# Optimization experiments

Measured on AMD Instinct MI355X. Metric: run time of the kernel, lower is better.

## Reference

```python
import jax, jax.numpy as jnp
import numpy as np
import math

B, S, D, H = 4, 2048, 512, 8
DK = D // H
EPS = 1e-6

def _xavier(key, shape):
    fan_in, fan_out = shape[1], shape[0]
    a = math.sqrt(6.0 / (fan_in + fan_out))
    return jax.random.uniform(key, shape, jnp.float32, -a, a)

def setup_inputs() -> dict:
    key = jax.random.key(0)
    ks = jax.random.split(key, 8)
    return {
        "x_q": jax.random.normal(ks[0], (B, S, D), jnp.float32),
        "x_k": jax.random.normal(ks[1], (B, S, D), jnp.float32),
        "Wq": _xavier(ks[2], (D, D)),
        "Wk": _xavier(ks[3], (D, D)),
        "Wv": _xavier(ks[4], (D, D)),
        "Wg": jnp.zeros((D, D), jnp.float32),      # gating weight init to 0
        "bg": jnp.ones((D,), jnp.float32),          # gating bias init to 1
        "Wo": _xavier(ks[5], (D, D)),
        "bo": jnp.zeros((D,), jnp.float32),
        "gamma": jnp.ones((D,), jnp.float32),
        "beta": jnp.zeros((D,), jnp.float32),
    }

def _ln(x, gamma, beta):
    mu = jnp.mean(x, axis=-1, keepdims=True)
    var = jnp.var(x, axis=-1, keepdims=True)
    return (x - mu) * jax.lax.rsqrt(var + EPS) * gamma + beta

def reference(x_q, x_k, Wq, Wk, Wv, Wg, bg, Wo, bo, gamma, beta):
    xq = _ln(x_q, gamma, beta)          # [B,S,D]
    xk = _ln(x_k, gamma, beta)
    q = xq @ Wq.T                        # nn.Linear: x @ W^T (no bias)
    k = xk @ Wk.T
    v = xk @ Wv.T
    q = q.reshape(B, S, H, DK)
    k = k.reshape(B, S, H, DK)
    v = v.reshape(B, S, H, DK)
    attn = jnp.einsum('bshd,bthd->bhst', q, k) / math.sqrt(DK)  # [B,H,S,S]
    attn = jax.nn.softmax(attn, axis=-1) * jax.nn.softmax(attn, axis=-2)
    out = jnp.einsum('bhst,bthd->bshd', attn, v).reshape(B, S, D)
    gate = jax.nn.sigmoid(xq @ Wg.T + bg)
    return (out * gate) @ Wo.T + bo
```

## Files before the change

kernel.cpp:

```cpp
#include <hip/hip_runtime.h>

#define BB 4
#define SS 2048
#define DD 512
#define HH 8
#define RR (BB * SS)
#define BH (BB * HH)

typedef unsigned short u16;
typedef unsigned int   u32;
typedef __attribute__((ext_vector_type(4))) float f32x4;
typedef __attribute__((ext_vector_type(8))) short bf16x8;

__device__ __forceinline__ float bf2f(u16 u) { return __uint_as_float(((u32)u) << 16); }
__device__ __forceinline__ u16 f2bf(float f) {
    u32 x = __float_as_uint(f);
    return (u16)((x + 0x7fffu + ((x >> 16) & 1u)) >> 16);
}
__device__ __forceinline__ bool is_bf16(const void* gamma) {
    return *(const u32*)gamma == 0x3F803F80u;
}
__device__ __forceinline__ float ldin(const void* p, size_t i, bool b16) {
    return b16 ? bf2f(((const u16*)p)[i]) : ((const float*)p)[i];
}
__device__ __forceinline__ float expc(float x) { return __expf(fminf(x, 60.f)); }

__global__ __launch_bounds__(256) void k_ln(
    const void* xq, const void* xk, const void* gamma, const void* beta,
    u16* __restrict__ lnq, u16* __restrict__ lnk, float* l_col)
{
    bool b16 = is_bf16(gamma);
    int row = blockIdx.x, tid = threadIdx.x;
    const void* x = blockIdx.y ? xk : xq;
    u16* o = blockIdx.y ? lnk : lnq;
    size_t base = (size_t)row * DD;

    if (blockIdx.y == 0 && row < 256) l_col[row * 256 + tid] = 0.f;

    float x0 = ldin(x, base + tid * 2, b16);
    float x1 = ldin(x, base + tid * 2 + 1, b16);
    float s = x0 + x1, ss = x0 * x0 + x1 * x1;
    for (int m = 1; m < 64; m <<= 1) { s += __shfl_xor(s, m); ss += __shfl_xor(ss, m); }
    __shared__ float ws4[4], wss4[4], mu_s, rs_s;
    int wv = tid >> 6;
    if ((tid & 63) == 0) { ws4[wv] = s; wss4[wv] = ss; }
    __syncthreads();
    if (tid == 0) {
        float S1 = ws4[0] + ws4[1] + ws4[2] + ws4[3];
        float S2 = wss4[0] + wss4[1] + wss4[2] + wss4[3];
        float mu = S1 / (float)DD;
        float var = S2 / (float)DD - mu * mu;
        mu_s = mu; rs_s = rsqrtf(fmaxf(var, 0.f) + 1e-6f);
    }
    __syncthreads();
    float mu = mu_s, rstd = rs_s;
    float g0 = ldin(gamma, tid * 2, b16), g1 = ldin(gamma, tid * 2 + 1, b16);
    float b0 = ldin(beta, tid * 2, b16),  b1 = ldin(beta, tid * 2 + 1, b16);
    o[base + tid * 2]     = f2bf((x0 - mu) * rstd * g0 + b0);
    o[base + tid * 2 + 1] = f2bf((x1 - mu) * rstd * g1 + b1);
}

__global__ __launch_bounds__(256) void k_proj4(
    const u16* __restrict__ lnq, const u16* __restrict__ lnk,
    const void* Wq, const void* Wk, const void* Wv, const void* Wg,
    const void* bg, const void* gamma,
    u16* __restrict__ qb, u16* __restrict__ kb,
    u16* __restrict__ vT, u16* __restrict__ gb)
{
    __shared__ __align__(16) u16 As[128][64];
    __shared__ __align__(16) u16 Bs[128][64];
    bool b16 = is_bf16(gamma);
    int which = blockIdx.z;
    const u16* A = (which <= 1) ? lnq : lnk;
    const void* W = (which == 0) ? Wq : (which == 1) ? Wg : (which == 2) ? Wk : Wv;
    u16* C = (which == 0) ? qb : (which == 1) ? gb : (which == 2) ? kb : vT;

    int tid = threadIdx.x;
    int lane = tid & 63, wave = tid >> 6;
    int r = lane & 15, q4 = lane >> 4;
    int m0 = blockIdx.y * 128, n0 = blockIdx.x * 128;
    int moff = (wave >> 1) * 64, noff = (wave & 1) * 64;
    const int K = DD, N = DD;

    f32x4 acc[4][4];
    for (int i = 0; i < 4; ++i)
        for (int j = 0; j < 4; ++j) acc[i][j] = (f32x4){0.f, 0.f, 0.f, 0.f};

    for (int k0 = 0; k0 < K; k0 += 64) {
        #pragma unroll
        for (int t = 0; t < 4; ++t) {
            int e = t * 2048 + tid * 8;
            int row = e >> 6, kk = e & 63;
            int ksw = kk ^ ((row & 7) * 8);
            *(uint4*)&As[row][ksw] = *(const uint4*)&A[(size_t)(m0 + row) * K + k0 + kk];
            if (b16) {
                *(uint4*)&Bs[row][ksw] =
                    *(const uint4*)&((const u16*)W)[(size_t)(n0 + row) * K + k0 + kk];
            } else {
                const float* wp = (const float*)W + (size_t)(n0 + row) * K + k0 + kk;
                float4 w0 = *(const float4*)wp;
                float4 w1 = *(const float4*)(wp + 4);
                ushort4 lo, hi;
                lo.x = f2bf(w0.x); lo.y = f2bf(w0.y); lo.z = f2bf(w0.z); lo.w = f2bf(w0.w);
                hi.x = f2bf(w1.x); hi.y = f2bf(w1.y); hi.z = f2bf(w1.z); hi.w = f2bf(w1.w);
                *(ushort4*)&Bs[row][ksw] = lo;
                *(ushort4*)&Bs[row][ksw + 4] = hi;
            }
        }
        __syncthreads();
        #pragma unroll
        for (int ksp = 0; ksp < 2; ++ksp) {
            int kb2 = ksp * 32 + q4 * 8;
            bf16x8 af[4], bfr[4];
            #pragma unroll
            for (int i = 0; i < 4; ++i) {
                int rowm = moff + i * 16 + r;
                af[i] = *(const bf16x8*)&As[rowm][kb2 ^ ((rowm & 7) * 8)];
                int rown = noff + i * 16 + r;
                bfr[i] = *(const bf16x8*)&Bs[rown][kb2 ^ ((rown & 7) * 8)];
            }
            #pragma unroll
            for (int i = 0; i < 4; ++i)
                #pragma unroll
                for (int j = 0; j < 4; ++j)
                    acc[i][j] = __builtin_amdgcn_mfma_f32_16x16x32_bf16(af[i], bfr[j], acc[i][j], 0, 0, 0);
        }
        __syncthreads();
    }

    if (which == 3) {
        int b = m0 >> 11;
        int sb = (m0 & 2047) + moff + q4 * 4;
        #pragma unroll
        for (int j = 0; j < 4; ++j) {
            int n = n0 + noff + j * 16 + r;
            int h = n >> 6, dkl = n & 63;
            size_t vbase = (((size_t)b * 8 + h) * 64 + dkl) * SS;
            #pragma unroll
            for (int i = 0; i < 4; ++i) {
                ushort4 wv;
                wv.x = f2bf(acc[i][j][0]); wv.y = f2bf(acc[i][j][1]);
                wv.z = f2bf(acc[i][j][2]); wv.w = f2bf(acc[i][j][3]);
                *(ushort4*)&C[vbase + sb + i * 16] = wv;
            }
        }
    } else {
        #pragma unroll
        for (int j = 0; j < 4; ++j) {
            int col = n0 + noff + j * 16 + r;
            float bj = (which == 1) ? ldin(bg, col, b16) : 0.f;
            #pragma unroll
            for (int i = 0; i < 4; ++i) {
                int rowb = m0 + moff + i * 16 + q4 * 4;
                #pragma unroll
                for (int g = 0; g < 4; ++g) {
                    float v = acc[i][j][g];
                    if (which == 1) v = 1.f / (1.f + expc(-(v + bj)));
                    C[(size_t)(rowb + g) * N + col] = f2bf(v);
                }
            }
        }
    }
}

__global__ __launch_bounds__(256) void k_sum(
    const u16* __restrict__ qm, const u16* __restrict__ km,
    float* __restrict__ l_row, float* __restrict__ l_col)
{
    __shared__ __align__(16) u16 Qs[64][64];
    __shared__ __align__(16) u16 Ks[128][64];
    __shared__ float colS[128];
    int tid = threadIdx.x, lane = tid & 63, wave = tid >> 6;
    int r = lane & 15, q4 = lane >> 4;
    int s0 = blockIdx.x * 64;
    int bh = blockIdx.y, b = bh >> 3, h = bh & 7;
    size_t hb = (size_t)b * SS * DD + (size_t)h * 64;

    #pragma unroll
    for (int t = 0; t < 2; ++t) {
        int e = t * 2048 + tid * 8;
        int row = e >> 6, kk = e & 63;
        *(uint4*)&Qs[row][kk ^ ((row & 7) * 8)] = *(const uint4*)&qm[hb + (size_t)(s0 + row) * DD + kk];
    }
    if (tid < 128) colS[tid] = 0.f;
    __syncthreads();

    int moff = wave * 16;
    bf16x8 aq[2];
    #pragma unroll
    for (int ksp = 0; ksp < 2; ++ksp) {
        int rowm = moff + r;
        aq[ksp] = *(const bf16x8*)&Qs[rowm][(ksp * 32 + q4 * 8) ^ ((rowm & 7) * 8)];
    }

    float rs[4] = {};
    for (int t0 = 0; t0 < SS; t0 += 128) {
        #pragma unroll
        for (int t = 0; t < 4; ++t) {
            int e = t * 2048 + tid * 8;
            int row = e >> 6, kk = e & 63;
            *(uint4*)&Ks[row][kk ^ ((row & 7) * 8)] = *(const uint4*)&km[hb + (size_t)(t0 + row) * DD + kk];
        }
        __syncthreads();

        f32x4 acc[8];
        for (int j = 0; j < 8; ++j) acc[j] = (f32x4){0.f, 0.f, 0.f, 0.f};
        #pragma unroll
        for (int ksp = 0; ksp < 2; ++ksp) {
            int kb2 = ksp * 32 + q4 * 8;
            bf16x8 bk[8];
            #pragma unroll
            for (int j = 0; j < 8; ++j) {
                int n = j * 16 + r;
                bk[j] = *(const bf16x8*)&Ks[n][kb2 ^ ((n & 7) * 8)];
            }
            #pragma unroll
            for (int j = 0; j < 8; ++j)
                acc[j] = __builtin_amdgcn_mfma_f32_16x16x32_bf16(aq[ksp], bk[j], acc[j], 0, 0, 0);
        }

        float cv[8];
        #pragma unroll
        for (int j = 0; j < 8; ++j) {
            cv[j] = 0.f;
            #pragma unroll
            for (int g = 0; g < 4; ++g) {
                float ev = expc(acc[j][g] * 0.125f);
                rs[g] += ev;
                cv[j] += ev;
            }
        }
        #pragma unroll
        for (int j = 0; j < 8; ++j) {
            float v = cv[j];
            v += __shfl_xor(v, 16); v += __shfl_xor(v, 32);
            if (q4 == 0) atomicAdd(&colS[j * 16 + r], v);
        }
        __syncthreads();
        if (tid < 128) {
            atomicAdd(&l_col[(size_t)bh * SS + t0 + tid], colS[tid]);
            colS[tid] = 0.f;
        }
        __syncthreads();
    }
    #pragma unroll
    for (int g = 0; g < 4; ++g) {
        float v = rs[g];
        v += __shfl_xor(v, 1); v += __shfl_xor(v, 2);
        v += __shfl_xor(v, 4); v += __shfl_xor(v, 8);
        if (r == 0) l_row[(size_t)bh * SS + s0 + moff + q4 * 4 + g] = v;
    }
}

__global__ void k_rcp(const float* __restrict__ l_row, const float* __restrict__ l_col,
                      float* __restrict__ inv_r, float* __restrict__ inv_c, int n)
{
    int i = blockIdx.x * blockDim.x + threadIdx.x;
    if (i < n) {
        inv_r[i] = 1.f / fmaxf(l_row[i], 1e-30f);
        inv_c[i] = 1.f / fmaxf(l_col[i], 1e-30f);
    }
}

__global__ __launch_bounds__(256) void k_pv(
    const u16* __restrict__ qm, const u16* __restrict__ km, const u16* __restrict__ vT,
    const float* __restrict__ inv_r, const float* __restrict__ inv_c,
    const u16* __restrict__ gate, u16* __restrict__ og)
{
    __shared__ __align__(16) u16 Ep[64][128];
    __shared__ __align__(16) u16 KV[8192];
    int tid = threadIdx.x, lane = tid & 63, wave = tid >> 6;
    int r = lane & 15, q4 = lane >> 4;
    int s0 = blockIdx.x * 64;
    int bh = blockIdx.y, b = bh >> 3, h = bh & 7;
    size_t hb = (size_t)b * SS * DD + (size_t)h * 64;
    int moff = wave * 16;

    #pragma unroll
    for (int t = 0; t < 2; ++t) {
        int e = t * 2048 + tid * 8;
        int row = e >> 6, kk = e & 63;
        *(uint4*)&Ep[row][kk ^ ((row & 7) * 8)] = *(const uint4*)&qm[hb + (size_t)(s0 + row) * DD + kk];
    }
    __syncthreads();
    bf16x8 aq[2];
    #pragma unroll
    for (int ksp = 0; ksp < 2; ++ksp) {
        int rowm = moff + r;
        aq[ksp] = *(const bf16x8*)&Ep[rowm][(ksp * 32 + q4 * 8) ^ ((rowm & 7) * 8)];
    }
    __syncthreads();

    f32x4 acco[4];
    for (int j = 0; j < 4; ++j) acco[j] = (f32x4){0.f, 0.f, 0.f, 0.f};

    for (int t0 = 0; t0 < SS; t0 += 128) {
        #pragma unroll
        for (int t = 0; t < 4; ++t) {
            int e = t * 2048 + tid * 8;
            int row = e >> 6, kk = e & 63;
            *(uint4*)&KV[row * 64 + (kk ^ ((row & 7) * 8))] =
                *(const uint4*)&km[hb + (size_t)(t0 + row) * DD + kk];
        }
        __syncthreads();

        f32x4 accs[8];
        for (int j = 0; j < 8; ++j) accs[j] = (f32x4){0.f, 0.f, 0.f, 0.f};
        #pragma unroll
        for (int ksp = 0; ksp < 2; ++ksp) {
            int kb2 = ksp * 32 + q4 * 8;
            bf16x8 bk[8];
            #pragma unroll
            for (int j = 0; j < 8; ++j) {
                int n = j * 16 + r;
                bk[j] = *(const bf16x8*)&KV[n * 64 + (kb2 ^ ((n & 7) * 8))];
            }
            #pragma unroll
            for (int j = 0; j < 8; ++j)
                accs[j] = __builtin_amdgcn_mfma_f32_16x16x32_bf16(aq[ksp], bk[j], accs[j], 0, 0, 0);
        }
        __syncthreads();

        #pragma unroll
        for (int c = 0; c < 4; ++c) {
            int e = c * 256 + tid;
            int row = e >> 4, tc = (e & 15) * 8;
            *(uint4*)&KV[row * 128 + (tc ^ ((row & 7) * 8))] =
                *(const uint4*)&vT[((size_t)bh * 64 + row) * SS + t0 + tc];
        }
        #pragma unroll
        for (int j = 0; j < 8; ++j) {
            float icj = inv_c[(size_t)bh * SS + t0 + j * 16 + r];
            int srow = moff + q4 * 4;
            #pragma unroll
            for (int g = 0; g < 4; ++g) {
                float pv = expc(accs[j][g] * 0.25f) * icj;
                int sl = srow + g, tl = j * 16 + r;
                Ep[sl][tl ^ ((sl & 7) * 8)] = f2bf(pv);
            }
        }
        __syncthreads();

        #pragma unroll
        for (int ksp = 0; ksp < 4; ++ksp) {
            int kb2 = ksp * 32 + q4 * 8;
            int sl = moff + r;
            bf16x8 ap = *(const bf16x8*)&Ep[sl][kb2 ^ ((sl & 7) * 8)];
            bf16x8 bv[4];
            #pragma unroll
            for (int j = 0; j < 4; ++j) {
                int n = j * 16 + r;
                bv[j] = *(const bf16x8*)&KV[n * 128 + (kb2 ^ ((n & 7) * 8))];
            }
            #pragma unroll
            for (int j = 0; j < 4; ++j)
                acco[j] = __builtin_amdgcn_mfma_f32_16x16x32_bf16(ap, bv[j], acco[j], 0, 0, 0);
        }
        __syncthreads();
    }

    #pragma unroll
    for (int g = 0; g < 4; ++g) {
        int srow = s0 + moff + q4 * 4 + g;
        float ir = inv_r[(size_t)bh * SS + srow];
        size_t ob = (size_t)b * SS * DD + (size_t)srow * DD + (size_t)h * 64;
        #pragma unroll
        for (int j = 0; j < 4; ++j) {
            int dk = j * 16 + r;
            og[ob + dk] = f2bf(acco[j][g] * ir * bf2f(gate[ob + dk]));
        }
    }
}

__global__ __launch_bounds__(256) void k_gemm_out(
    const u16* __restrict__ A, const void* W, const void* gamma,
    float* __restrict__ Cf, const void* bias)
{
    __shared__ __align__(16) u16 As[128][64];
    __shared__ __align__(16) u16 Bs[128][64];
    bool b16 = is_bf16(gamma);
    int tid = threadIdx.x;
    int lane = tid & 63, wave = tid >> 6;
    int r = lane & 15, q4 = lane >> 4;
    int m0 = blockIdx.y * 128, n0 = blockIdx.x * 128;
    int moff = (wave >> 1) * 64, noff = (wave & 1) * 64;
    const int K = DD, N = DD;

    f32x4 acc[4][4];
    for (int i = 0; i < 4; ++i)
        for (int j = 0; j < 4; ++j) acc[i][j] = (f32x4){0.f, 0.f, 0.f, 0.f};

    for (int k0 = 0; k0 < K; k0 += 64) {
        #pragma unroll
        for (int t = 0; t < 4; ++t) {
            int e = t * 2048 + tid * 8;
            int row = e >> 6, kk = e & 63;
            int ksw = kk ^ ((row & 7) * 8);
            *(uint4*)&As[row][ksw] = *(const uint4*)&A[(size_t)(m0 + row) * K + k0 + kk];
            if (b16) {
                *(uint4*)&Bs[row][ksw] =
                    *(const uint4*)&((const u16*)W)[(size_t)(n0 + row) * K + k0 + kk];
            } else {
                const float* wp = (const float*)W + (size_t)(n0 + row) * K + k0 + kk;
                float4 w0 = *(const float4*)wp;
                float4 w1 = *(const float4*)(wp + 4);
                ushort4 lo, hi;
                lo.x = f2bf(w0.x); lo.y = f2bf(w0.y); lo.z = f2bf(w0.z); lo.w = f2bf(w0.w);
                hi.x = f2bf(w1.x); hi.y = f2bf(w1.y); hi.z = f2bf(w1.z); hi.w = f2bf(w1.w);
                *(ushort4*)&Bs[row][ksw] = lo;
                *(ushort4*)&Bs[row][ksw + 4] = hi;
            }
        }
        __syncthreads();
        #pragma unroll
        for (int ksp = 0; ksp < 2; ++ksp) {
            int kb2 = ksp * 32 + q4 * 8;
            bf16x8 af[4], bfr[4];
            #pragma unroll
            for (int i = 0; i < 4; ++i) {
                int rowm = moff + i * 16 + r;
                af[i] = *(const bf16x8*)&As[rowm][kb2 ^ ((rowm & 7) * 8)];
                int rown = noff + i * 16 + r;
                bfr[i] = *(const bf16x8*)&Bs[rown][kb2 ^ ((rown & 7) * 8)];
            }
            #pragma unroll
            for (int i = 0; i < 4; ++i)
                #pragma unroll
                for (int j = 0; j < 4; ++j)
                    acc[i][j] = __builtin_amdgcn_mfma_f32_16x16x32_bf16(af[i], bfr[j], acc[i][j], 0, 0, 0);
        }
        __syncthreads();
    }
    #pragma unroll
    for (int j = 0; j < 4; ++j) {
        int col = n0 + noff + j * 16 + r;
        float bj = ldin(bias, col, b16);
        #pragma unroll
        for (int i = 0; i < 4; ++i) {
            int rowb = m0 + moff + i * 16 + q4 * 4;
            #pragma unroll
            for (int g = 0; g < 4; ++g) {
                float v = acc[i][j][g] + bj;
                size_t idx = (size_t)(rowb + g) * N + col;
                if (b16) ((u16*)Cf)[idx] = f2bf(v);
                else     Cf[idx] = v;
            }
        }
    }
}

extern "C" void kernel_launch(void* const* d_in, const int* in_sizes, int n_in,
                              void* d_out, int out_size, void* d_ws, size_t ws_size,
                              hipStream_t stream)
{
    const void* x_q   = d_in[0];
    const void* x_k   = d_in[1];
    const void* Wq    = d_in[2];
    const void* Wk    = d_in[3];
    const void* Wv    = d_in[4];
    const void* Wg    = d_in[5];
    const void* bg    = d_in[6];
    const void* Wo    = d_in[7];
    const void* bo    = d_in[8];
    const void* gamma = d_in[9];
    const void* beta  = d_in[10];

    char* base = (char*)d_ws;
    u16* lnq = (u16*)(base);
    u16* lnk = (u16*)(base + (size_t) 8 * 1024 * 1024);
    u16* qb  = (u16*)(base + (size_t)16 * 1024 * 1024);
    u16* kb  = (u16*)(base + (size_t)24 * 1024 * 1024);
    u16* gb  = (u16*)(base + (size_t)32 * 1024 * 1024);
    float* l_row = (float*)(base + (size_t)40 * 1024 * 1024);
    float* l_col = (float*)(base + (size_t)40 * 1024 * 1024 + 262144);
    float* inv_r = (float*)(base + (size_t)40 * 1024 * 1024 + 524288);
    float* inv_c = (float*)(base + (size_t)40 * 1024 * 1024 + 786432);
    u16* vT = (u16*)d_out;
    u16* og = lnk;

    k_ln<<<dim3(RR, 2), 256, 0, stream>>>(x_q, x_k, gamma, beta, lnq, lnk, l_col);

    k_proj4<<<dim3(4, 64, 4), 256, 0, stream>>>(lnq, lnk, Wq, Wk, Wv, Wg, bg, gamma,
                                                qb, kb, vT, gb);

    k_sum<<<dim3(SS / 64, BH), 256, 0, stream>>>(qb, kb, l_row, l_col);
    k_rcp<<<dim3(BH * SS / 256), 256, 0, stream>>>(l_row, l_col, inv_r, inv_c, BH * SS);
    k_pv<<<dim3(SS / 64, BH), 256, 0, stream>>>(qb, kb, vT, inv_r, inv_c, gb, og);

    k_gemm_out<<<dim3(4, 64), 256, 0, stream>>>(og, Wo, gamma, (float*)d_out, bo);
}
```

Measured before the change: 355.5 us.

## Split key range across waves with register-resident Q and barrier-free K prefetch

Both attention kernels now keep the block's 64 query rows in registers and give each wave its own 32-key slice of every 128-key step. K (and V in k_pv) are loaded straight from global memory into registers with double buffering instead of through shared memory, which removes the per-iteration barriers. In k_sum, column sums are reduced with shuffles and sent to global atomics, and row sums are combined through a small shared buffer. In k_pv, each wave builds its P tile in a private LDS slab and keeps partial outputs for all 64 rows, which are merged at the end with shared-memory atomics before applying the gate. This trades more global atomics, more accumulator registers and an LDS atomic reduction for fewer block synchronisations and shared-memory round trips.

```diff
diff --git a/kernel.cpp b/kernel.cpp
--- a/kernel.cpp
+++ b/kernel.cpp
@@ -167,89 +167,79 @@
     const u16* __restrict__ qm, const u16* __restrict__ km,
     float* __restrict__ l_row, float* __restrict__ l_col)
 {
-    __shared__ __align__(16) u16 Qs[64][64];
-    __shared__ __align__(16) u16 Ks[128][64];
-    __shared__ float colS[128];
-    int tid = threadIdx.x, lane = tid & 63, wave = tid >> 6;
+    __shared__ float rowbuf[64];
+    int tid = threadIdx.x, lane = tid & 63, w = tid >> 6;
     int r = lane & 15, q4 = lane >> 4;
     int s0 = blockIdx.x * 64;
     int bh = blockIdx.y, b = bh >> 3, h = bh & 7;
-    size_t hb = (size_t)b * SS * DD + (size_t)h * 64;
-
-    #pragma unroll
-    for (int t = 0; t < 2; ++t) {
-        int e = t * 2048 + tid * 8;
-        int row = e >> 6, kk = e & 63;
-        *(uint4*)&Qs[row][kk ^ ((row & 7) * 8)] = *(const uint4*)&qm[hb + (size_t)(s0 + row) * DD + kk];
-    }
-    if (tid < 128) colS[tid] = 0.f;
-    __syncthreads();
-
-    int moff = wave * 16;
-    bf16x8 aq[2];
-    #pragma unroll
-    for (int ksp = 0; ksp < 2; ++ksp) {
-        int rowm = moff + r;
-        aq[ksp] = *(const bf16x8*)&Qs[rowm][(ksp * 32 + q4 * 8) ^ ((rowm & 7) * 8)];
-    }
-
-    float rs[4] = {};
-    for (int t0 = 0; t0 < SS; t0 += 128) {
-        #pragma unroll
-        for (int t = 0; t < 4; ++t) {
-            int e = t * 2048 + tid * 8;
-            int row = e >> 6, kk = e & 63;
-            *(uint4*)&Ks[row][kk ^ ((row & 7) * 8)] = *(const uint4*)&km[hb + (size_t)(t0 + row) * DD + kk];
-        }
-        __syncthreads();
-
-        f32x4 acc[8];
-        for (int j = 0; j < 8; ++j) acc[j] = (f32x4){0.f, 0.f, 0.f, 0.f};
-        #pragma unroll
-        for (int ksp = 0; ksp < 2; ++ksp) {
-            int kb2 = ksp * 32 + q4 * 8;
-            bf16x8 bk[8];
-            #pragma unroll
-            for (int j = 0; j < 8; ++j) {
-                int n = j * 16 + r;
-                bk[j] = *(const bf16x8*)&Ks[n][kb2 ^ ((n & 7) * 8)];
-            }
-            #pragma unroll
-            for (int j = 0; j < 8; ++j)
-                acc[j] = __builtin_amdgcn_mfma_f32_16x16x32_bf16(aq[ksp], bk[j], acc[j], 0, 0, 0);
-        }
-
-        float cv[8];
-        #pragma unroll
-        for (int j = 0; j < 8; ++j) {
-            cv[j] = 0.f;
+    const u16* qh = qm + (size_t)b * SS * DD + (size_t)h * 64;
+    const u16* kh = km + (size_t)b * SS * DD + (size_t)h * 64;
+    int w32 = w * 32;
+
+    if (tid < 64) rowbuf[tid] = 0.f;
+    __syncthreads();
+
+    bf16x8 bq[4][2];
+    #pragma unroll
+    for (int n = 0; n < 4; ++n)
+        #pragma unroll
+        for (int ks = 0; ks < 2; ++ks)
+            bq[n][ks] = *(const bf16x8*)&qh[(size_t)(s0 + n * 16 + r) * DD + ks * 32 + q4 * 8];
+
+    float rs[4] = {0.f, 0.f, 0.f, 0.f};
+
+    bf16x8 akA[2][2], akB[2][2];
+    auto LOADK = [&](bf16x8 (&dst)[2][2], int tb) {
+        #pragma unroll
+        for (int m = 0; m < 2; ++m)
+            #pragma unroll
+            for (int ks = 0; ks < 2; ++ks)
+                dst[m][ks] = *(const bf16x8*)&kh[(size_t)(tb + m * 16 + r) * DD + ks * 32 + q4 * 8];
+    };
+    auto STEP = [&](int it, bf16x8 (&cur)[2][2], bf16x8 (&nxt)[2][2]) {
+        if (it < 15) LOADK(nxt, (it + 1) * 128 + w32);
+        f32x4 accs[2][4];
+        #pragma unroll
+        for (int m = 0; m < 2; ++m)
+            #pragma unroll
+            for (int n = 0; n < 4; ++n) accs[m][n] = (f32x4){0.f, 0.f, 0.f, 0.f};
+        #pragma unroll
+        for (int ks = 0; ks < 2; ++ks)
+            #pragma unroll
+            for (int m = 0; m < 2; ++m)
+                #pragma unroll
+                for (int n = 0; n < 4; ++n)
+                    accs[m][n] = __builtin_amdgcn_mfma_f32_16x16x32_bf16(cur[m][ks], bq[n][ks], accs[m][n], 0, 0, 0);
+        int t0w = it * 128 + w32;
+        #pragma unroll
+        for (int m = 0; m < 2; ++m)
             #pragma unroll
             for (int g = 0; g < 4; ++g) {
-                float ev = expc(acc[j][g] * 0.125f);
-                rs[g] += ev;
-                cv[j] += ev;
-            }
-        }
-        #pragma unroll
-        for (int j = 0; j < 8; ++j) {
-            float v = cv[j];
-            v += __shfl_xor(v, 16); v += __shfl_xor(v, 32);
-            if (q4 == 0) atomicAdd(&colS[j * 16 + r], v);
-        }
-        __syncthreads();
-        if (tid < 128) {
-            atomicAdd(&l_col[(size_t)bh * SS + t0 + tid], colS[tid]);
-            colS[tid] = 0.f;
-        }
-        __syncthreads();
-    }
-    #pragma unroll
-    for (int g = 0; g < 4; ++g) {
-        float v = rs[g];
-        v += __shfl_xor(v, 1); v += __shfl_xor(v, 2);
-        v += __shfl_xor(v, 4); v += __shfl_xor(v, 8);
-        if (r == 0) l_row[(size_t)bh * SS + s0 + moff + q4 * 4 + g] = v;
-    }
+                float e0 = expc(accs[m][0][g] * 0.125f);
+                float e1 = expc(accs[m][1][g] * 0.125f);
+                float e2 = expc(accs[m][2][g] * 0.125f);
+                float e3 = expc(accs[m][3][g] * 0.125f);
+                rs[0] += e0; rs[1] += e1; rs[2] += e2; rs[3] += e3;
+                float c4 = (e0 + e1) + (e2 + e3);
+                c4 += __shfl_xor(c4, 1); c4 += __shfl_xor(c4, 2);
+                c4 += __shfl_xor(c4, 4); c4 += __shfl_xor(c4, 8);
+                if (r == 0)
+                    atomicAdd(&l_col[(size_t)bh * SS + t0w + m * 16 + q4 * 4 + g], c4);
+            }
+    };
+    LOADK(akA, w32);
+    for (int it = 0; it < 16; it += 2) {
+        STEP(it,     akA, akB);
+        STEP(it + 1, akB, akA);
+    }
+    #pragma unroll
+    for (int n = 0; n < 4; ++n) {
+        float v = rs[n];
+        v += __shfl_xor(v, 16); v += __shfl_xor(v, 32);
+        if (q4 == 0) atomicAdd(&rowbuf[n * 16 + r], v);
+    }
+    __syncthreads();
+    if (tid < 64) l_row[(size_t)bh * SS + s0 + tid] = rowbuf[tid];
 }
 
 __global__ void k_rcp(const float* __restrict__ l_row, const float* __restrict__ l_col,
@@ -267,107 +257,124 @@
     const float* __restrict__ inv_r, const float* __restrict__ inv_c,
     const u16* __restrict__ gate, u16* __restrict__ og)
 {
-    __shared__ __align__(16) u16 Ep[64][128];
-    __shared__ __align__(16) u16 KV[8192];
-    int tid = threadIdx.x, lane = tid & 63, wave = tid >> 6;
+    __shared__ __align__(16) u16 Plds[4][64][32];
+    __shared__ float Obuf[64][66];
+    int tid = threadIdx.x, lane = tid & 63, w = tid >> 6;
     int r = lane & 15, q4 = lane >> 4;
     int s0 = blockIdx.x * 64;
     int bh = blockIdx.y, b = bh >> 3, h = bh & 7;
-    size_t hb = (size_t)b * SS * DD + (size_t)h * 64;
-    int moff = wave * 16;
-
-    #pragma unroll
-    for (int t = 0; t < 2; ++t) {
-        int e = t * 2048 + tid * 8;
-        int row = e >> 6, kk = e & 63;
-        *(uint4*)&Ep[row][kk ^ ((row & 7) * 8)] = *(const uint4*)&qm[hb + (size_t)(s0 + row) * DD + kk];
-    }
-    __syncthreads();
-    bf16x8 aq[2];
-    #pragma unroll
-    for (int ksp = 0; ksp < 2; ++ksp) {
-        int rowm = moff + r;
-        aq[ksp] = *(const bf16x8*)&Ep[rowm][(ksp * 32 + q4 * 8) ^ ((rowm & 7) * 8)];
-    }
-    __syncthreads();
-
-    f32x4 acco[4];
-    for (int j = 0; j < 4; ++j) acco[j] = (f32x4){0.f, 0.f, 0.f, 0.f};
-
-    for (int t0 = 0; t0 < SS; t0 += 128) {
-        #pragma unroll
-        for (int t = 0; t < 4; ++t) {
-            int e = t * 2048 + tid * 8;
-            int row = e >> 6, kk = e & 63;
-            *(uint4*)&KV[row * 64 + (kk ^ ((row & 7) * 8))] =
-                *(const uint4*)&km[hb + (size_t)(t0 + row) * DD + kk];
-        }
-        __syncthreads();
-
-        f32x4 accs[8];
-        for (int j = 0; j < 8; ++j) accs[j] = (f32x4){0.f, 0.f, 0.f, 0.f};
-        #pragma unroll
-        for (int ksp = 0; ksp < 2; ++ksp) {
-            int kb2 = ksp * 32 + q4 * 8;
-            bf16x8 bk[8];
-            #pragma unroll
-            for (int j = 0; j < 8; ++j) {
-                int n = j * 16 + r;
-                bk[j] = *(const bf16x8*)&KV[n * 64 + (kb2 ^ ((n & 7) * 8))];
-            }
-            #pragma unroll
-            for (int j = 0; j < 8; ++j)
-                accs[j] = __builtin_amdgcn_mfma_f32_16x16x32_bf16(aq[ksp], bk[j], accs[j], 0, 0, 0);
-        }
-        __syncthreads();
-
-        #pragma unroll
-        for (int c = 0; c < 4; ++c) {
-            int e = c * 256 + tid;
-            int row = e >> 4, tc = (e & 15) * 8;
-            *(uint4*)&KV[row * 128 + (tc ^ ((row & 7) * 8))] =
-                *(const uint4*)&vT[((size_t)bh * 64 + row) * SS + t0 + tc];
-        }
-        #pragma unroll
-        for (int j = 0; j < 8; ++j) {
-            float icj = inv_c[(size_t)bh * SS + t0 + j * 16 + r];
-            int srow = moff + q4 * 4;
-            #pragma unroll
-            for (int g = 0; g < 4; ++g) {
-                float pv = expc(accs[j][g] * 0.25f) * icj;
-                int sl = srow + g, tl = j * 16 + r;
-                Ep[sl][tl ^ ((sl & 7) * 8)] = f2bf(pv);
-            }
-        }
-        __syncthreads();
-
-        #pragma unroll
-        for (int ksp = 0; ksp < 4; ++ksp) {
-            int kb2 = ksp * 32 + q4 * 8;
-            int sl = moff + r;
-            bf16x8 ap = *(const bf16x8*)&Ep[sl][kb2 ^ ((sl & 7) * 8)];
-            bf16x8 bv[4];
-            #pragma unroll
-            for (int j = 0; j < 4; ++j) {
-                int n = j * 16 + r;
-                bv[j] = *(const bf16x8*)&KV[n * 128 + (kb2 ^ ((n & 7) * 8))];
-            }
+    const u16* qh = qm + (size_t)b * SS * DD + (size_t)h * 64;
+    const u16* kh = km + (size_t)b * SS * DD + (size_t)h * 64;
+    const u16* vh = vT + (size_t)bh * 64 * SS;
+    size_t icb = (size_t)bh * SS;
+    int w32 = w * 32;
+    int rsw = (r & 3) * 8, q48 = q4 * 8;
+    u16* myP = &Plds[w][0][0];
+
+    for (int i = tid; i < 64 * 66; i += 256) ((float*)Obuf)[i] = 0.f;
+    __syncthreads();
+
+    bf16x8 bq[4][2];
+    #pragma unroll
+    for (int n = 0; n < 4; ++n)
+        #pragma unroll
+        for (int ks = 0; ks < 2; ++ks)
+            bq[n][ks] = *(const bf16x8*)&qh[(size_t)(s0 + n * 16 + r) * DD + ks * 32 + q4 * 8];
+
+    f32x4 acco[4][4];
+    #pragma unroll
+    for (int ms = 0; ms < 4; ++ms)
+        #pragma unroll
+        for (int j = 0; j < 4; ++j) acco[ms][j] = (f32x4){0.f, 0.f, 0.f, 0.f};
+
+    bf16x8 akA[2][2], akB[2][2];
+    auto LOADK = [&](bf16x8 (&dst)[2][2], int tb) {
+        #pragma unroll
+        for (int m = 0; m < 2; ++m)
+            #pragma unroll
+            for (int ks = 0; ks < 2; ++ks)
+                dst[m][ks] = *(const bf16x8*)&kh[(size_t)(tb + m * 16 + r) * DD + ks * 32 + q4 * 8];
+    };
+    auto STEP = [&](int it, bf16x8 (&cur)[2][2], bf16x8 (&nxt)[2][2]) {
+        int t0w = it * 128 + w32;
+        bf16x8 bv[4];
+        #pragma unroll
+        for (int j = 0; j < 4; ++j)
+            bv[j] = *(const bf16x8*)&vh[(size_t)(j * 16 + r) * SS + t0w + q48];
+        float4 ic0 = *(const float4*)&inv_c[icb + t0w + q4 * 4];
+        float4 ic1 = *(const float4*)&inv_c[icb + t0w + 16 + q4 * 4];
+        if (it < 15) LOADK(nxt, t0w + 128);
+
+        f32x4 accs[2][4];
+        #pragma unroll
+        for (int m = 0; m < 2; ++m)
+            #pragma unroll
+            for (int n = 0; n < 4; ++n) accs[m][n] = (f32x4){0.f, 0.f, 0.f, 0.f};
+        #pragma unroll
+        for (int ks = 0; ks < 2; ++ks)
+            #pragma unroll
+            for (int m = 0; m < 2; ++m)
+                #pragma unroll
+                for (int n = 0; n < 4; ++n)
+                    accs[m][n] = __builtin_amdgcn_mfma_f32_16x16x32_bf16(cur[m][ks], bq[n][ks], accs[m][n], 0, 0, 0);
+
+        #pragma unroll
+        for (int m = 0; m < 2; ++m) {
+            float4 ic = m ? ic1 : ic0;
+            #pragma unroll
+            for (int n = 0; n < 4; ++n) {
+                float p0 = expc(accs[m][n][0] * 0.25f) * ic.x;
+                float p1 = expc(accs[m][n][1] * 0.25f) * ic.y;
+                float p2 = expc(accs[m][n][2] * 0.25f) * ic.z;
+                float p3 = expc(accs[m][n][3] * 0.25f) * ic.w;
+                u32 w0, w1;
+                asm("v_cvt_pk_bf16_f32 %0, %1, %2" : "=v"(w0) : "v"(p0), "v"(p1));
+                asm("v_cvt_pk_bf16_f32 %0, %1, %2" : "=v"(w1) : "v"(p2), "v"(p3));
+                int row = n * 16 + r;
+                int colb = (m * 16 + q4 * 4) ^ rsw;
+                *(u32*)&myP[row * 32 + colb]     = w0;
+                *(u32*)&myP[row * 32 + colb + 2] = w1;
+            }
+        }
+
+        #pragma unroll
+        for (int ms = 0; ms < 4; ++ms) {
+            bf16x8 pa = *(const bf16x8*)&myP[(ms * 16 + r) * 32 + (q48 ^ rsw)];
             #pragma unroll
             for (int j = 0; j < 4; ++j)
-                acco[j] = __builtin_amdgcn_mfma_f32_16x16x32_bf16(ap, bv[j], acco[j], 0, 0, 0);
-        }
-        __syncthreads();
-    }
-
-    #pragma unroll
-    for (int g = 0; g < 4; ++g) {
-        int srow = s0 + moff + q4 * 4 + g;
+                acco[ms][j] = __builtin_amdgcn_mfma_f32_16x16x32_bf16(pa, bv[j], acco[ms][j], 0, 0, 0);
+        }
+    };
+
+    LOADK(akA, w32);
+    for (int it = 0; it < 16; it += 2) {
+        STEP(it,     akA, akB);
+        STEP(it + 1, akB, akA);
+    }
+
+    #pragma unroll
+    for (int ms = 0; ms < 4; ++ms)
+        #pragma unroll
+        for (int j = 0; j < 4; ++j)
+            #pragma unroll
+            for (int g = 0; g < 4; ++g)
+                atomicAdd(&Obuf[ms * 16 + q4 * 4 + g][j * 16 + r], acco[ms][j][g]);
+    __syncthreads();
+
+    {
+        int s = tid >> 2, c0 = (tid & 3) * 16;
+        int srow = s0 + s;
         float ir = inv_r[(size_t)bh * SS + srow];
-        size_t ob = (size_t)b * SS * DD + (size_t)srow * DD + (size_t)h * 64;
-        #pragma unroll
-        for (int j = 0; j < 4; ++j) {
-            int dk = j * 16 + r;
-            og[ob + dk] = f2bf(acco[j][g] * ir * bf2f(gate[ob + dk]));
+        size_t ob = (size_t)b * SS * DD + (size_t)srow * DD + (size_t)h * 64 + c0;
+        #pragma unroll
+        for (int c = 0; c < 16; c += 4) {
+            ushort4 gv = *(const ushort4*)&gate[ob + c];
+            ushort4 wv;
+            wv.x = f2bf(Obuf[s][c0 + c + 0] * ir * bf2f(gv.x));
+            wv.y = f2bf(Obuf[s][c0 + c + 1] * ir * bf2f(gv.y));
+            wv.z = f2bf(Obuf[s][c0 + c + 2] * ir * bf2f(gv.z));
+            wv.w = f2bf(Obuf[s][c0 + c + 3] * ir * bf2f(gv.w));
+            *(ushort4*)&og[ob + c] = wv;
         }
     }
 }
```

After: 463.5 us. +30.4%, slower.

## Fold score scale into Q, pre-scale V by column sums, batch column atomics

Applied to the files above, without the earlier changes.

Folds the 1/sqrt(dk) factor into the Q projection epilogue and swaps the exponentials for exp2 with premultiplied log2e constants. Column-sum reduction now accumulates in a full-length shared array per block and flushes to global once at the end, which removes the two barriers and the global atomics in every tile iteration. The column-softmax normalisation moves out of the PV loop into a new kernel that scales V^T in place. The PV kernel also swaps the MFMA operands so each lane writes packed bf16 pairs, using v_cvt_pk_bf16_f32, instead of scalar stores. This adds an extra launch and an extra pass over V, and uses 8KB more shared memory in k_sum, which may reduce occupancy.

```diff
diff --git a/kernel.cpp b/kernel.cpp
--- a/kernel.cpp
+++ b/kernel.cpp
@@ -24,6 +24,12 @@
     return b16 ? bf2f(((const u16*)p)[i]) : ((const float*)p)[i];
 }
 __device__ __forceinline__ float expc(float x) { return __expf(fminf(x, 60.f)); }
+__device__ __forceinline__ float e2sum(float x) {
+    return __builtin_amdgcn_exp2f(fminf(x * 1.44269504f, 86.5617f));
+}
+__device__ __forceinline__ float e2pv(float x) {
+    return __builtin_amdgcn_exp2f(fminf(x * 2.88539008f, 86.5617f));
+}
 
 __global__ __launch_bounds__(256) void k_ln(
     const void* xq, const void* xk, const void* gamma, const void* beta,
@@ -156,6 +162,7 @@
                 for (int g = 0; g < 4; ++g) {
                     float v = acc[i][j][g];
                     if (which == 1) v = 1.f / (1.f + expc(-(v + bj)));
+                    else if (which == 0) v *= 0.125f;
                     C[(size_t)(rowb + g) * N + col] = f2bf(v);
                 }
             }
@@ -169,7 +176,7 @@
 {
     __shared__ __align__(16) u16 Qs[64][64];
     __shared__ __align__(16) u16 Ks[128][64];
-    __shared__ float colS[128];
+    __shared__ float colS[SS];
     int tid = threadIdx.x, lane = tid & 63, wave = tid >> 6;
     int r = lane & 15, q4 = lane >> 4;
     int s0 = blockIdx.x * 64;
@@ -182,7 +189,7 @@
         int row = e >> 6, kk = e & 63;
         *(uint4*)&Qs[row][kk ^ ((row & 7) * 8)] = *(const uint4*)&qm[hb + (size_t)(s0 + row) * DD + kk];
     }
-    if (tid < 128) colS[tid] = 0.f;
+    for (int i = tid; i < SS; i += 256) colS[i] = 0.f;
     __syncthreads();
 
     int moff = wave * 16;
@@ -219,27 +226,16 @@
                 acc[j] = __builtin_amdgcn_mfma_f32_16x16x32_bf16(aq[ksp], bk[j], acc[j], 0, 0, 0);
         }
 
-        float cv[8];
         #pragma unroll
         for (int j = 0; j < 8; ++j) {
-            cv[j] = 0.f;
-            #pragma unroll
-            for (int g = 0; g < 4; ++g) {
-                float ev = expc(acc[j][g] * 0.125f);
-                rs[g] += ev;
-                cv[j] += ev;
-            }
-        }
-        #pragma unroll
-        for (int j = 0; j < 8; ++j) {
-            float v = cv[j];
+            float e0 = e2sum(acc[j][0]);
+            float e1 = e2sum(acc[j][1]);
+            float e2 = e2sum(acc[j][2]);
+            float e3 = e2sum(acc[j][3]);
+            rs[0] += e0; rs[1] += e1; rs[2] += e2; rs[3] += e3;
+            float v = (e0 + e1) + (e2 + e3);
             v += __shfl_xor(v, 16); v += __shfl_xor(v, 32);
-            if (q4 == 0) atomicAdd(&colS[j * 16 + r], v);
-        }
-        __syncthreads();
-        if (tid < 128) {
-            atomicAdd(&l_col[(size_t)bh * SS + t0 + tid], colS[tid]);
-            colS[tid] = 0.f;
+            if (q4 == 0) atomicAdd(&colS[t0 + j * 16 + r], v);
         }
         __syncthreads();
     }
@@ -250,21 +246,41 @@
         v += __shfl_xor(v, 4); v += __shfl_xor(v, 8);
         if (r == 0) l_row[(size_t)bh * SS + s0 + moff + q4 * 4 + g] = v;
     }
-}
-
-__global__ void k_rcp(const float* __restrict__ l_row, const float* __restrict__ l_col,
-                      float* __restrict__ inv_r, float* __restrict__ inv_c, int n)
+    for (int i = tid; i < SS; i += 256)
+        atomicAdd(&l_col[(size_t)bh * SS + i], colS[i]);
+}
+
+__global__ void k_rcp(const float* __restrict__ l_row, float* __restrict__ inv_r, int n)
 {
     int i = blockIdx.x * blockDim.x + threadIdx.x;
-    if (i < n) {
-        inv_r[i] = 1.f / fmaxf(l_row[i], 1e-30f);
-        inv_c[i] = 1.f / fmaxf(l_col[i], 1e-30f);
-    }
+    if (i < n) inv_r[i] = 1.f / fmaxf(l_row[i], 1e-30f);
+}
+
+__global__ __launch_bounds__(256) void k_vscale(
+    u16* __restrict__ vT, const float* __restrict__ l_col)
+{
+    int row = blockIdx.x;
+    int bh = row >> 6;
+    int t = threadIdx.x * 8;
+    size_t base = (size_t)row * SS + t;
+    const float* lc = &l_col[(size_t)bh * SS + t];
+    bf16x8 v = *(const bf16x8*)&vT[base];
+    float4 c0 = *(const float4*)lc;
+    float4 c1 = *(const float4*)(lc + 4);
+    float s[8] = {1.f / fmaxf(c0.x, 1e-30f), 1.f / fmaxf(c0.y, 1e-30f),
+                  1.f / fmaxf(c0.z, 1e-30f), 1.f / fmaxf(c0.w, 1e-30f),
+                  1.f / fmaxf(c1.x, 1e-30f), 1.f / fmaxf(c1.y, 1e-30f),
+                  1.f / fmaxf(c1.z, 1e-30f), 1.f / fmaxf(c1.w, 1e-30f)};
+    bf16x8 o;
+    #pragma unroll
+    for (int e = 0; e < 8; ++e)
+        o[e] = (short)f2bf(bf2f((u16)v[e]) * s[e]);
+    *(bf16x8*)&vT[base] = o;
 }
 
 __global__ __launch_bounds__(256) void k_pv(
     const u16* __restrict__ qm, const u16* __restrict__ km, const u16* __restrict__ vT,
-    const float* __restrict__ inv_r, const float* __restrict__ inv_c,
+    const float* __restrict__ inv_r,
     const u16* __restrict__ gate, u16* __restrict__ og)
 {
     __shared__ __align__(16) u16 Ep[64][128];
@@ -294,6 +310,8 @@
     f32x4 acco[4];
     for (int j = 0; j < 4; ++j) acco[j] = (f32x4){0.f, 0.f, 0.f, 0.f};
 
+    int sl = moff + r, swz = (sl & 7) * 8;
+
     for (int t0 = 0; t0 < SS; t0 += 128) {
         #pragma unroll
         for (int t = 0; t < 4; ++t) {
@@ -305,19 +323,20 @@
         __syncthreads();
 
         f32x4 accs[8];
-        for (int j = 0; j < 8; ++j) accs[j] = (f32x4){0.f, 0.f, 0.f, 0.f};
+        #pragma unroll
+        for (int m = 0; m < 8; ++m) accs[m] = (f32x4){0.f, 0.f, 0.f, 0.f};
         #pragma unroll
         for (int ksp = 0; ksp < 2; ++ksp) {
             int kb2 = ksp * 32 + q4 * 8;
-            bf16x8 bk[8];
-            #pragma unroll
-            for (int j = 0; j < 8; ++j) {
-                int n = j * 16 + r;
-                bk[j] = *(const bf16x8*)&KV[n * 64 + (kb2 ^ ((n & 7) * 8))];
-            }
-            #pragma unroll
-            for (int j = 0; j < 8; ++j)
-                accs[j] = __builtin_amdgcn_mfma_f32_16x16x32_bf16(aq[ksp], bk[j], accs[j], 0, 0, 0);
+            bf16x8 ak[8];
+            #pragma unroll
+            for (int m = 0; m < 8; ++m) {
+                int n = m * 16 + r;
+                ak[m] = *(const bf16x8*)&KV[n * 64 + (kb2 ^ ((n & 7) * 8))];
+            }
+            #pragma unroll
+            for (int m = 0; m < 8; ++m)
+                accs[m] = __builtin_amdgcn_mfma_f32_16x16x32_bf16(ak[m], aq[ksp], accs[m], 0, 0, 0);
         }
         __syncthreads();
 
@@ -329,23 +348,23 @@
                 *(const uint4*)&vT[((size_t)bh * 64 + row) * SS + t0 + tc];
         }
         #pragma unroll
-        for (int j = 0; j < 8; ++j) {
-            float icj = inv_c[(size_t)bh * SS + t0 + j * 16 + r];
-            int srow = moff + q4 * 4;
-            #pragma unroll
-            for (int g = 0; g < 4; ++g) {
-                float pv = expc(accs[j][g] * 0.25f) * icj;
-                int sl = srow + g, tl = j * 16 + r;
-                Ep[sl][tl ^ ((sl & 7) * 8)] = f2bf(pv);
-            }
+        for (int m = 0; m < 8; ++m) {
+            float p0 = e2pv(accs[m][0]);
+            float p1 = e2pv(accs[m][1]);
+            float p2 = e2pv(accs[m][2]);
+            float p3 = e2pv(accs[m][3]);
+            u32 w0, w1;
+            asm("v_cvt_pk_bf16_f32 %0, %1, %2" : "=v"(w0) : "v"(p0), "v"(p1));
+            asm("v_cvt_pk_bf16_f32 %0, %1, %2" : "=v"(w1) : "v"(p2), "v"(p3));
+            uint2 pr; pr.x = w0; pr.y = w1;
+            *(uint2*)&Ep[sl][(m * 16 + q4 * 4) ^ swz] = pr;
         }
         __syncthreads();
 
         #pragma unroll
         for (int ksp = 0; ksp < 4; ++ksp) {
             int kb2 = ksp * 32 + q4 * 8;
-            int sl = moff + r;
-            bf16x8 ap = *(const bf16x8*)&Ep[sl][kb2 ^ ((sl & 7) * 8)];
+            bf16x8 ap = *(const bf16x8*)&Ep[sl][kb2 ^ swz];
             bf16x8 bv[4];
             #pragma unroll
             for (int j = 0; j < 4; ++j) {
@@ -474,7 +493,6 @@
     float* l_row = (float*)(base + (size_t)40 * 1024 * 1024);
     float* l_col = (float*)(base + (size_t)40 * 1024 * 1024 + 262144);
     float* inv_r = (float*)(base + (size_t)40 * 1024 * 1024 + 524288);
-    float* inv_c = (float*)(base + (size_t)40 * 1024 * 1024 + 786432);
     u16* vT = (u16*)d_out;
     u16* og = lnk;
 
@@ -484,8 +502,9 @@
                                                 qb, kb, vT, gb);
 
     k_sum<<<dim3(SS / 64, BH), 256, 0, stream>>>(qb, kb, l_row, l_col);
-    k_rcp<<<dim3(BH * SS / 256), 256, 0, stream>>>(l_row, l_col, inv_r, inv_c, BH * SS);
-    k_pv<<<dim3(SS / 64, BH), 256, 0, stream>>>(qb, kb, vT, inv_r, inv_c, gb, og);
+    k_rcp<<<dim3(BH * SS / 256), 256, 0, stream>>>(l_row, inv_r, BH * SS);
+    k_vscale<<<dim3(BH * 64), 256, 0, stream>>>(vT, l_col);
+    k_pv<<<dim3(SS / 64, BH), 256, 0, stream>>>(qb, kb, vT, inv_r, gb, og);
 
     k_gemm_out<<<dim3(4, 64), 256, 0, stream>>>(og, Wo, gamma, (float*)d_out, bo);
 }
```

Result: faster. 334.0 us (-6.1%).
